# Kernel optimization log

Measured on AMD Instinct MI355X. Metric: run time of the kernel, lower is better.

## Reference

```python
import jax, jax.numpy as jnp
import numpy as np

DEGREE = 3
N_BASIS = 16


def _clamped_knots(n_basis, degree):
    # Clamped uniform knot vector on [0, 1]: degree+1 repeated knots at each end.
    n_interior = n_basis - degree - 1
    interior = np.linspace(0.0, 1.0, n_interior + 2)[1:-1]
    knots = np.concatenate([np.zeros(degree + 1), interior, np.ones(degree + 1)])
    return jnp.asarray(knots, dtype=jnp.float32)


def bspline_basis(x, degree=DEGREE, n_basis=N_BASIS):
    # Cox-de Boor recursion, vectorized over all leading dims of x.
    # x: (...,) in [0,1] -> (..., n_basis)
    t = _clamped_knots(n_basis, degree)
    n_knots = n_basis + degree + 1
    xe = jnp.clip(x, 0.0, 1.0 - 1e-6)[..., None]
    B = ((xe >= t[:-1]) & (xe < t[1:])).astype(x.dtype)  # (..., n_knots-1)
    for p in range(1, degree + 1):
        dl = t[p:n_knots - 1] - t[:n_knots - 1 - p]
        dr = t[p + 1:n_knots] - t[1:n_knots - p]
        left = jnp.where(dl > 0, (xe - t[:n_knots - 1 - p]) / jnp.where(dl > 0, dl, 1.0), 0.0)
        right = jnp.where(dr > 0, (t[p + 1:n_knots] - xe) / jnp.where(dr > 0, dr, 1.0), 0.0)
        B = left * B[..., :-1] + right * B[..., 1:]
    return B  # (..., n_basis)


def _kl(cm, lv):
    # KL(N(cm, exp(lv)) || N(0, 1)) summed over all edges/coeffs (prior_scale = 1).
    var = jnp.exp(lv)
    return 0.5 * jnp.sum(var + cm * cm - 1.0 - lv)


def _layer(x, cm, lv):
    # x: (B, in); cm, lv: (out, in, n_basis)
    basis = bspline_basis(x)  # (B, in, n_basis)
    out = jnp.einsum('bik,oik->bo', basis, cm)  # fused per-edge weighted sum
    return out, _kl(cm, lv)


def setup_inputs() -> dict:
    key = jax.random.key(0)
    ks = jax.random.split(key, 4)
    B = 8192
    sizes = [256, 512, 512, 256]
    nb = N_BASIS
    inp = {"x": jax.random.uniform(ks[0], (B, sizes[0]), dtype=jnp.float32)}
    for i in range(3):
        inp[f"cm{i}"] = 0.1 * jax.random.normal(ks[1 + i], (sizes[i + 1], sizes[i], nb), dtype=jnp.float32)
        inp[f"lv{i}"] = -2.0 * jnp.ones((sizes[i + 1], sizes[i], nb), dtype=jnp.float32)
    return inp


def reference(x, cm0, lv0, cm1, lv1, cm2, lv2):
    out = x
    kl = jnp.zeros((), x.dtype)
    for cm, lv in ((cm0, lv0), (cm1, lv1), (cm2, lv2)):
        out, k = _layer(out, cm, lv)
        kl = kl + k
    return out, kl
```

## Files before the change

kernel.cpp:

```cpp
#include <hip/hip_runtime.h>
#include <hip/hip_bf16.h>


typedef __attribute__((ext_vector_type(8))) _Float16 f16x8;
typedef __attribute__((ext_vector_type(4))) float float4v;
typedef unsigned short ushort_t;

#define GLOBAL_AS __attribute__((address_space(1)))
#define LDS_AS __attribute__((address_space(3)))

__device__ __forceinline__ void async_copy16(const void* g, void* l) {
  __builtin_amdgcn_global_load_lds((const GLOBAL_AS unsigned int*)g,
                                   (LDS_AS unsigned int*)l, 16, 0, 0);
}

__device__ __forceinline__ ushort_t f2h(float f) {
  _Float16 h = (_Float16)f;
  return *(ushort_t*)&h;
}
__device__ __forceinline__ float h2f(ushort_t u) {
  return (float)*(_Float16*)&u;
}

__device__ __forceinline__ void bspline_w4(float x, int& k0, float w[4]) {
  const float XMAX = 1.0f - 1e-6f;
  float xe = fminf(fmaxf(x, 0.0f), XMAX);
  int cell = (int)(xe * 13.0f);
  cell = cell > 12 ? 12 : cell;
  k0 = cell;
  int j = cell + 3;
  const float s = 1.0f / 13.0f;
  int cjm2 = max(j - 5, 0);
  int cjm1 = max(j - 4, 0);
  int cj   = j - 3;
  int cj1  = j - 2;
  int cj2  = min(j - 1, 13);
  int cj3  = min(j, 13);
  float tjm2 = cjm2 * s, tjm1 = cjm1 * s, tj = cj * s;
  float tj1 = cj1 * s, tj2 = cj2 * s, tj3 = cj3 * s;
  float left1 = xe - tj, left2 = xe - tjm1, left3 = xe - tjm2;
  float right1 = tj1 - xe, right2 = tj2 - xe, right3 = tj3 - xe;
#define INV3(d) ((d) == 1 ? 13.0f : ((d) == 2 ? 6.5f : (13.0f / 3.0f)))
  float i10 = INV3(cj1 - cj);
  float i20 = INV3(cj1 - cjm1), i21 = INV3(cj2 - cj);
  float i30 = INV3(cj1 - cjm2), i31 = INV3(cj2 - cjm1), i32 = INV3(cj3 - cj);
#undef INV3
  float temp = i10;
  float N0 = right1 * temp;
  float N1 = left1 * temp;
  temp = N0 * i20;
  N0 = right1 * temp;
  float saved = left2 * temp;
  temp = N1 * i21;
  N1 = saved + right2 * temp;
  float N2 = left1 * temp;
  temp = N0 * i30;
  N0 = right1 * temp;
  saved = left3 * temp;
  temp = N1 * i31;
  N1 = saved + right2 * temp;
  saved = left2 * temp;
  temp = N2 * i32;
  N2 = saved + right3 * temp;
  float N3 = left1 * temp;
  w[0] = N0; w[1] = N1; w[2] = N2; w[3] = N3;
}

template <bool SPLIT_A>
__global__ __launch_bounds__(256) void kan_layer(
    const float* __restrict__ act, const ushort_t* __restrict__ cmh,
    float* __restrict__ outp, int IN, int OUT) {
  const int K = IN * 16;
  __shared__ ushort_t Ah[128 * 72];
  __shared__ ushort_t Al[SPLIT_A ? 128 * 72 : 1];
  __shared__ ushort_t Bh[128 * 64];

  const int tid = threadIdx.x;
  const int lane = tid & 63;
  const int wv = tid >> 6;
  const int wm = wv >> 1, wn = wv & 1;
  const int quad = lane >> 4, l15 = lane & 15;
  const int b0 = blockIdx.x * 128;
  const int n0 = blockIdx.y * 128;

  float4v acc[4][4];
#pragma unroll
  for (int a = 0; a < 4; a++)
#pragma unroll
    for (int b = 0; b < 4; b++) acc[a][b] = (float4v)0.0f;

  const int gm = tid >> 1;
  const int gip = (tid & 1) * 2;

  const int lrow = lane >> 3;
  const int lcol8 = (lane & 7) ^ lrow;

  const int nsteps = K / 64;
  const int Z = gridDim.z;
  const int chunk = nsteps / Z;
  const int kbeg = blockIdx.z * chunk;
  const int kend = min(kbeg + chunk, nsteps);
  for (int kstep = kbeg; kstep < kend; ++kstep) {
    const int i0 = kstep * 4;
    __syncthreads();

#pragma unroll
    for (int j = 0; j < 4; ++j) {
      int w = wv * 4 + j;
      size_t goff = (size_t)(n0 + w * 8 + lrow) * K + (size_t)kstep * 64 + lcol8 * 8;
      async_copy16(&cmh[goff], &Bh[w * 512]);
    }

    {
      const float2 xv = *(const float2*)&act[(size_t)(b0 + gm) * IN + i0 + gip];
      uint4 z; z.x = z.y = z.z = z.w = 0u;
      ushort_t* arow_h = &Ah[gm * 72 + gip * 16];
      ((uint4*)arow_h)[0] = z; ((uint4*)arow_h)[1] = z;
      ((uint4*)arow_h)[2] = z; ((uint4*)arow_h)[3] = z;
      ushort_t* arow_l = nullptr;
      if (SPLIT_A) {
        arow_l = &Al[gm * 72 + gip * 16];
        ((uint4*)arow_l)[0] = z; ((uint4*)arow_l)[1] = z;
        ((uint4*)arow_l)[2] = z; ((uint4*)arow_l)[3] = z;
      }
#pragma unroll
      for (int e = 0; e < 2; ++e) {
        int k0; float w[4];
        bspline_w4(e == 0 ? xv.x : xv.y, k0, w);
#pragma unroll
        for (int t = 0; t < 4; ++t) {
          ushort_t h = f2h(w[t]);
          arow_h[e * 16 + k0 + t] = h;
          if (SPLIT_A)
            arow_l[e * 16 + k0 + t] = f2h(w[t] - h2f(h));
        }
      }
    }
    __syncthreads();

#pragma unroll
    for (int ks = 0; ks < 2; ++ks) {
      f16x8 ah[4], al[4], bh[4];
#pragma unroll
      for (int mt = 0; mt < 4; ++mt) {
        int off = (wm * 64 + mt * 16 + l15) * 72 + ks * 32 + quad * 8;
        ah[mt] = *(const f16x8*)&Ah[off];
        if (SPLIT_A) al[mt] = *(const f16x8*)&Al[off];
      }
#pragma unroll
      for (int nt = 0; nt < 4; ++nt) {
        int n = wn * 64 + nt * 16 + l15;
        int slot = (ks * 4 + quad) ^ (n & 7);
        bh[nt] = *(const f16x8*)&Bh[n * 64 + slot * 8];
      }
#pragma unroll
      for (int mt = 0; mt < 4; ++mt)
#pragma unroll
        for (int nt = 0; nt < 4; ++nt) {
          if (SPLIT_A)
            acc[mt][nt] = __builtin_amdgcn_mfma_f32_16x16x32_f16(al[mt], bh[nt], acc[mt][nt], 0, 0, 0);
          acc[mt][nt] = __builtin_amdgcn_mfma_f32_16x16x32_f16(ah[mt], bh[nt], acc[mt][nt], 0, 0, 0);
        }
    }
  }

#pragma unroll
  for (int mt = 0; mt < 4; ++mt)
#pragma unroll
    for (int nt = 0; nt < 4; ++nt) {
      int col = n0 + wn * 64 + nt * 16 + l15;
#pragma unroll
      for (int r = 0; r < 4; ++r) {
        int row = b0 + wm * 64 + mt * 16 + quad * 4 + r;
        atomicAdd(&outp[(size_t)row * OUT + col], acc[mt][nt][r]);
      }
    }
}

__global__ __launch_bounds__(256) void kl_convert(
    const float* __restrict__ cm, const float* __restrict__ lv,
    ushort_t* __restrict__ ch, long long n, float* __restrict__ klout) {
  long long i = (long long)blockIdx.x * blockDim.x + threadIdx.x;
  const long long stride = (long long)gridDim.x * blockDim.x;
  float s = 0.0f;
  for (; i < n; i += stride) {
    float c = cm[i], l = lv[i];
    ch[i] = f2h(c);
    s += 0.5f * (__expf(l) + c * c - 1.0f - l);
  }
#pragma unroll
  for (int o = 32; o > 0; o >>= 1) s += __shfl_down(s, o, 64);
  __shared__ float red[4];
  int wv = threadIdx.x >> 6;
  if ((threadIdx.x & 63) == 0) red[wv] = s;
  __syncthreads();
  if (threadIdx.x == 0)
    atomicAdd(klout, red[0] + red[1] + red[2] + red[3]);
}

extern "C" void kernel_launch(void* const* d_in, const int* in_sizes, int n_in,
                              void* d_out, int out_size, void* d_ws, size_t ws_size,
                              hipStream_t stream) {
  const float* x   = (const float*)d_in[0];
  const float* cm0 = (const float*)d_in[1];
  const float* lv0 = (const float*)d_in[2];
  const float* cm1 = (const float*)d_in[3];
  const float* lv1 = (const float*)d_in[4];
  const float* cm2 = (const float*)d_in[5];
  const float* lv2 = (const float*)d_in[6];

  float* out = (float*)d_out;
  float* klp = out + (size_t)8192 * 256;

  char* ws = (char*)d_ws;
  float*    act1 = (float*)(ws);
  float*    act2 = (float*)(ws + ((size_t)16 << 20));
  ushort_t* c0h  = (ushort_t*)(ws + ((size_t)32 << 20));
  ushort_t* c1h  = (ushort_t*)(ws + ((size_t)36 << 20));
  ushort_t* c2h  = (ushort_t*)(ws + ((size_t)44 << 20));

  hipMemsetAsync(ws, 0, (size_t)32 << 20, stream);
  hipMemsetAsync(d_out, 0, (size_t)out_size * sizeof(float), stream);

  kl_convert<<<2048, 256, 0, stream>>>(cm0, lv0, c0h, 512LL * 256 * 16, klp);
  kl_convert<<<2048, 256, 0, stream>>>(cm1, lv1, c1h, 512LL * 512 * 16, klp);
  kl_convert<<<2048, 256, 0, stream>>>(cm2, lv2, c2h, 256LL * 512 * 16, klp);

  kan_layer<true ><<<dim3(64, 4, 4), 256, 0, stream>>>(x,    c0h, act1, 256, 512);
  kan_layer<false><<<dim3(64, 4, 4), 256, 0, stream>>>(act1, c1h, act2, 512, 512);
  kan_layer<false><<<dim3(64, 2, 8), 256, 0, stream>>>(act2, c2h, out,  512, 256);
}
```

Baseline: 538.9 us.

## Pre-swizzle weights into MFMA fragment layout and load B directly to registers

The fp16 conversion kernel now writes the coefficient tensor in a tiled layout where each 16-row by 8-k group is contiguous, so every wavefront can load its MFMA B fragments straight from global memory into registers. This removes the LDS staging buffer for B and its async copies. The global loads and the B-spline evaluation are issued before the barrier so they overlap the previous step's work. Launch bounds now request two blocks per SIMD. The cost is more register pressure and less B reuse through LDS, since both wm wavefronts fetch the same fragments from global/L2.

```diff
diff --git a/kernel.cpp b/kernel.cpp
--- a/kernel.cpp
+++ b/kernel.cpp
@@ -5,14 +5,6 @@
 typedef __attribute__((ext_vector_type(8))) _Float16 f16x8;
 typedef __attribute__((ext_vector_type(4))) float float4v;
 typedef unsigned short ushort_t;
-
-#define GLOBAL_AS __attribute__((address_space(1)))
-#define LDS_AS __attribute__((address_space(3)))
-
-__device__ __forceinline__ void async_copy16(const void* g, void* l) {
-  __builtin_amdgcn_global_load_lds((const GLOBAL_AS unsigned int*)g,
-                                   (LDS_AS unsigned int*)l, 16, 0, 0);
-}
 
 __device__ __forceinline__ ushort_t f2h(float f) {
   _Float16 h = (_Float16)f;
@@ -36,7 +28,8 @@
   int cj1  = j - 2;
   int cj2  = min(j - 1, 13);
   int cj3  = min(j, 13);
-  float tjm2 = cjm2 * s, tjm1 = cjm1 * s, tj = cj * s;
+  float tjm1 = cjm1 * s, tj = cj * s;
+  float tjm2 = cjm2 * s;
   float tj1 = cj1 * s, tj2 = cj2 * s, tj3 = cj3 * s;
   float left1 = xe - tj, left2 = xe - tjm1, left3 = xe - tjm2;
   float right1 = tj1 - xe, right2 = tj2 - xe, right3 = tj3 - xe;
@@ -67,13 +60,13 @@
 }
 
 template <bool SPLIT_A>
-__global__ __launch_bounds__(256) void kan_layer(
-    const float* __restrict__ act, const ushort_t* __restrict__ cmh,
+__global__ __launch_bounds__(256, 2) void kan_layer(
+    const float* __restrict__ act, const ushort_t* __restrict__ Bsw,
     float* __restrict__ outp, int IN, int OUT) {
   const int K = IN * 16;
+  const int KC = K >> 3;
   __shared__ ushort_t Ah[128 * 72];
   __shared__ ushort_t Al[SPLIT_A ? 128 * 72 : 1];
-  __shared__ ushort_t Bh[128 * 64];
 
   const int tid = threadIdx.x;
   const int lane = tid & 63;
@@ -82,6 +75,7 @@
   const int quad = lane >> 4, l15 = lane & 15;
   const int b0 = blockIdx.x * 128;
   const int n0 = blockIdx.y * 128;
+  const int tbase = (n0 >> 4) + wn * 4;
 
   float4v acc[4][4];
 #pragma unroll
@@ -92,47 +86,48 @@
   const int gm = tid >> 1;
   const int gip = (tid & 1) * 2;
 
-  const int lrow = lane >> 3;
-  const int lcol8 = (lane & 7) ^ lrow;
-
   const int nsteps = K / 64;
-  const int Z = gridDim.z;
-  const int chunk = nsteps / Z;
+  const int chunk = nsteps / gridDim.z;
   const int kbeg = blockIdx.z * chunk;
-  const int kend = min(kbeg + chunk, nsteps);
+  const int kend = kbeg + chunk;
   for (int kstep = kbeg; kstep < kend; ++kstep) {
     const int i0 = kstep * 4;
+
+    const float2 xv = *(const float2*)&act[(size_t)(b0 + gm) * IN + i0 + gip];
+    f16x8 bfrag[2][4];
+#pragma unroll
+    for (int ks = 0; ks < 2; ++ks)
+#pragma unroll
+      for (int nt = 0; nt < 4; ++nt) {
+        size_t eoff = (((size_t)(tbase + nt)) * KC + kstep * 8 + ks * 4) * 128
+                      + lane * 8;
+        bfrag[ks][nt] = *(const f16x8*)&Bsw[eoff];
+      }
+
+    int k0a, k0b; float wa[4], wb[4];
+    bspline_w4(xv.x, k0a, wa);
+    bspline_w4(xv.y, k0b, wb);
+
     __syncthreads();
 
-#pragma unroll
-    for (int j = 0; j < 4; ++j) {
-      int w = wv * 4 + j;
-      size_t goff = (size_t)(n0 + w * 8 + lrow) * K + (size_t)kstep * 64 + lcol8 * 8;
-      async_copy16(&cmh[goff], &Bh[w * 512]);
-    }
-
     {
-      const float2 xv = *(const float2*)&act[(size_t)(b0 + gm) * IN + i0 + gip];
       uint4 z; z.x = z.y = z.z = z.w = 0u;
       ushort_t* arow_h = &Ah[gm * 72 + gip * 16];
       ((uint4*)arow_h)[0] = z; ((uint4*)arow_h)[1] = z;
       ((uint4*)arow_h)[2] = z; ((uint4*)arow_h)[3] = z;
-      ushort_t* arow_l = nullptr;
+#pragma unroll
+      for (int t = 0; t < 4; ++t) {
+        arow_h[k0a + t] = f2h(wa[t]);
+        arow_h[16 + k0b + t] = f2h(wb[t]);
+      }
       if (SPLIT_A) {
-        arow_l = &Al[gm * 72 + gip * 16];
+        ushort_t* arow_l = &Al[gm * 72 + gip * 16];
         ((uint4*)arow_l)[0] = z; ((uint4*)arow_l)[1] = z;
         ((uint4*)arow_l)[2] = z; ((uint4*)arow_l)[3] = z;
-      }
-#pragma unroll
-      for (int e = 0; e < 2; ++e) {
-        int k0; float w[4];
-        bspline_w4(e == 0 ? xv.x : xv.y, k0, w);
 #pragma unroll
         for (int t = 0; t < 4; ++t) {
-          ushort_t h = f2h(w[t]);
-          arow_h[e * 16 + k0 + t] = h;
-          if (SPLIT_A)
-            arow_l[e * 16 + k0 + t] = f2h(w[t] - h2f(h));
+          arow_l[k0a + t] = f2h(wa[t] - h2f(f2h(wa[t])));
+          arow_l[16 + k0b + t] = f2h(wb[t] - h2f(f2h(wb[t])));
         }
       }
     }
@@ -140,7 +135,7 @@
 
 #pragma unroll
     for (int ks = 0; ks < 2; ++ks) {
-      f16x8 ah[4], al[4], bh[4];
+      f16x8 ah[4], al[4];
 #pragma unroll
       for (int mt = 0; mt < 4; ++mt) {
         int off = (wm * 64 + mt * 16 + l15) * 72 + ks * 32 + quad * 8;
@@ -148,18 +143,12 @@
         if (SPLIT_A) al[mt] = *(const f16x8*)&Al[off];
       }
 #pragma unroll
-      for (int nt = 0; nt < 4; ++nt) {
-        int n = wn * 64 + nt * 16 + l15;
-        int slot = (ks * 4 + quad) ^ (n & 7);
-        bh[nt] = *(const f16x8*)&Bh[n * 64 + slot * 8];
-      }
-#pragma unroll
       for (int mt = 0; mt < 4; ++mt)
 #pragma unroll
         for (int nt = 0; nt < 4; ++nt) {
           if (SPLIT_A)
-            acc[mt][nt] = __builtin_amdgcn_mfma_f32_16x16x32_f16(al[mt], bh[nt], acc[mt][nt], 0, 0, 0);
-          acc[mt][nt] = __builtin_amdgcn_mfma_f32_16x16x32_f16(ah[mt], bh[nt], acc[mt][nt], 0, 0, 0);
+            acc[mt][nt] = __builtin_amdgcn_mfma_f32_16x16x32_f16(al[mt], bfrag[ks][nt], acc[mt][nt], 0, 0, 0);
+          acc[mt][nt] = __builtin_amdgcn_mfma_f32_16x16x32_f16(ah[mt], bfrag[ks][nt], acc[mt][nt], 0, 0, 0);
         }
     }
   }
@@ -179,17 +168,31 @@
 
 __global__ __launch_bounds__(256) void kl_convert(
     const float* __restrict__ cm, const float* __restrict__ lv,
-    ushort_t* __restrict__ ch, long long n, float* __restrict__ klout) {
+    ushort_t* __restrict__ bsw, int G ,
+    long long ngroups, float* __restrict__ klout) {
   long long i = (long long)blockIdx.x * blockDim.x + threadIdx.x;
   const long long stride = (long long)gridDim.x * blockDim.x;
   float s = 0.0f;
-  for (; i < n; i += stride) {
-    float c = cm[i], l = lv[i];
-    ch[i] = f2h(c);
-    s += 0.5f * (__expf(l) + c * c - 1.0f - l);
+  for (; i < ngroups; i += stride) {
+    int o = (int)(i / G);
+    int kc = (int)(i - (long long)o * G);
+    const float* cp = &cm[i * 8];
+    const float* lp = &lv[i * 8];
+    unsigned pk[4];
+#pragma unroll
+    for (int t = 0; t < 4; ++t) {
+      float c0 = cp[2 * t], c1 = cp[2 * t + 1];
+      float l0 = lp[2 * t], l1 = lp[2 * t + 1];
+      pk[t] = (unsigned)f2h(c0) | ((unsigned)f2h(c1) << 16);
+      s += 0.5f * (__expf(l0) + c0 * c0 - 1.0f - l0);
+      s += 0.5f * (__expf(l1) + c1 * c1 - 1.0f - l1);
+    }
+    uint4 v; v.x = pk[0]; v.y = pk[1]; v.z = pk[2]; v.w = pk[3];
+    size_t doff = (((size_t)(o >> 4) * G + kc) * 16 + (o & 15)) * 8;
+    *(uint4*)&bsw[doff] = v;
   }
 #pragma unroll
-  for (int o = 32; o > 0; o >>= 1) s += __shfl_down(s, o, 64);
+  for (int off = 32; off > 0; off >>= 1) s += __shfl_down(s, off, 64);
   __shared__ float red[4];
   int wv = threadIdx.x >> 6;
   if ((threadIdx.x & 63) == 0) red[wv] = s;
@@ -215,18 +218,18 @@
   char* ws = (char*)d_ws;
   float*    act1 = (float*)(ws);
   float*    act2 = (float*)(ws + ((size_t)16 << 20));
-  ushort_t* c0h  = (ushort_t*)(ws + ((size_t)32 << 20));
-  ushort_t* c1h  = (ushort_t*)(ws + ((size_t)36 << 20));
-  ushort_t* c2h  = (ushort_t*)(ws + ((size_t)44 << 20));
+  ushort_t* b0sw = (ushort_t*)(ws + ((size_t)32 << 20));
+  ushort_t* b1sw = (ushort_t*)(ws + ((size_t)36 << 20));
+  ushort_t* b2sw = (ushort_t*)(ws + ((size_t)44 << 20));
 
   hipMemsetAsync(ws, 0, (size_t)32 << 20, stream);
   hipMemsetAsync(d_out, 0, (size_t)out_size * sizeof(float), stream);
 
-  kl_convert<<<2048, 256, 0, stream>>>(cm0, lv0, c0h, 512LL * 256 * 16, klp);
-  kl_convert<<<2048, 256, 0, stream>>>(cm1, lv1, c1h, 512LL * 512 * 16, klp);
-  kl_convert<<<2048, 256, 0, stream>>>(cm2, lv2, c2h, 256LL * 512 * 16, klp);
-
-  kan_layer<true ><<<dim3(64, 4, 4), 256, 0, stream>>>(x,    c0h, act1, 256, 512);
-  kan_layer<false><<<dim3(64, 4, 4), 256, 0, stream>>>(act1, c1h, act2, 512, 512);
-  kan_layer<false><<<dim3(64, 2, 8), 256, 0, stream>>>(act2, c2h, out,  512, 256);
-}
+  kl_convert<<<2048, 256, 0, stream>>>(cm0, lv0, b0sw, 256 * 2, 512LL * 256 * 2, klp);
+  kl_convert<<<2048, 256, 0, stream>>>(cm1, lv1, b1sw, 512 * 2, 512LL * 512 * 2, klp);
+  kl_convert<<<2048, 256, 0, stream>>>(cm2, lv2, b2sw, 512 * 2, 256LL * 512 * 2, klp);
+
+  kan_layer<true ><<<dim3(64, 4, 4), 256, 0, stream>>>(x,    b0sw, act1, 256, 512);
+  kan_layer<false><<<dim3(64, 4, 4), 256, 0, stream>>>(act1, b1sw, act2, 512, 512);
+  kan_layer<false><<<dim3(64, 2, 8), 256, 0, stream>>>(act2, b2sw, out,  512, 256);
+}
```

After: 486.9 us. 1.11x faster.
